# Performance work log

Hardware: AMD Instinct MI355X
Metric: run time of the kernel (lower is better)

## Reference

```python
import jax, jax.numpy as jnp
import numpy as np

DIM = 256
K = 255
PAD = K // 2  # 127, 'same' padding


def _dwconv(x, w, b, pad_h, pad_w):
    # x: [N, C, H, W]; w: [C, 1, kh, kw] (OIHW with feature_group_count=C)
    y = jax.lax.conv_general_dilated(
        x, w,
        window_strides=(1, 1),
        padding=((pad_h, pad_h), (pad_w, pad_w)),
        dimension_numbers=("NCHW", "OIHW", "NCHW"),
        feature_group_count=x.shape[1],
    )
    return y + b[None, :, None, None]


def setup_inputs() -> dict:
    key = jax.random.key(0)
    k1, k2, k3, k4, k5 = jax.random.split(key, 5)
    x = jax.random.normal(k1, (10, DIM, 128, 128), dtype=jnp.float32)
    # depthwise weights, scaled like torch's kaiming-uniform fan_in=K
    scale = 1.0 / np.sqrt(K)
    wh = jax.random.uniform(k2, (DIM, 1, K, 1), jnp.float32, -scale, scale)
    bh = jax.random.uniform(k3, (DIM,), jnp.float32, -scale, scale)
    ww = jax.random.uniform(k4, (DIM, 1, 1, K), jnp.float32, -scale, scale)
    bw = jax.random.uniform(k5, (DIM,), jnp.float32, -scale, scale)
    return {"x": x, "wh": wh, "bh": bh, "ww": ww, "bw": bw}


def reference(x, wh, bh, ww, bw):
    # conv_h: (K,1) depthwise conv, padding (K//2, 0)
    x = _dwconv(x, wh, bh, PAD, 0)
    # conv_w: (1,K) depthwise conv, padding (0, K//2)
    x = _dwconv(x, ww, bw, 0, PAD)
    return x
```

## Files before the change

### kernel.cpp

```cpp
#include <hip/hip_runtime.h>

#define HW 128
#define KTAPS 255
#define DIMC 256

typedef short short8 __attribute__((ext_vector_type(8)));
typedef float f32x16 __attribute__((ext_vector_type(16)));

__device__ __forceinline__ short f2bf(float f) {
    return __builtin_bit_cast(short, (__bf16)f);
}
__device__ __forceinline__ int pad16(int c) { return c + (c >> 3); }

__device__ __forceinline__ void bar_lds() {
    asm volatile("s_waitcnt lgkmcnt(0)" ::: "memory");
    __builtin_amdgcn_s_barrier();
}


__global__ __launch_bounds__(1024, 4)
void sep_conv255_mfma(const float* __restrict__ x,
                      const float* __restrict__ wh,
                      const float* __restrict__ bh,
                      const float* __restrict__ ww,
                      const float* __restrict__ bw,
                      float* __restrict__ out,
                      int nslices) {
    __shared__ __align__(16) short Px[2][2304 * 8];
    __shared__ __align__(16) short Py[2304 * 8];
    __shared__ __align__(16) short WB[1792 * 8];

    const int c    = blockIdx.x;
    const int tid  = threadIdx.x;
    const int lane = tid & 63;
    const int wv   = tid >> 6;
    const int wm   = wv >> 2;
    const int wn   = wv & 3;
    const int s31  = lane & 31;

    const float* __restrict__ whc = wh + c * KTAPS;
    const float* __restrict__ wwc = ww + c * KTAPS;
    const float bhv = bh[c];
    const float bwv = bw[c];

    const int xn   = tid & 127;
    const int xg   = tid >> 7;
    const int xch0 = (((xn >> 5) << 3) + xg) * 64 + (xn & 31);
    const size_t xoff = (size_t)(xg << 4) * HW + xn;

    float xv[16];
    {
        const float* xs = x + (size_t)c * (HW * HW);
#pragma unroll
        for (int i = 0; i < 16; ++i) xv[i] = xs[xoff + i * HW];
    }
#pragma unroll
    for (int i = 0; i < 2; ++i) {
        const int ch = tid + (i << 10);
        if (ch < 1792) {
            const int isB = (ch >= 896);
            const int lc  = ch & 63;
            const int t   = (ch >> 6) - (isB ? 14 : 0);
            const float* ws = isB ? wwc : whc;
            const float* wp = ws + (31 + (t << 4) + ((lc >> 5) << 3) - (lc & 31));
            short8 v;
#pragma unroll
            for (int j = 0; j < 8; ++j) v[j] = f2bf(wp[j]);
            *reinterpret_cast<short8*>(&WB[ch * 8]) = v;
        }
    }
#pragma unroll
    for (int hh = 0; hh < 2; ++hh) {
        short8 v;
#pragma unroll
        for (int j = 0; j < 8; ++j) v[j] = f2bf(xv[(hh << 3) + j]);
        *reinterpret_cast<short8*>(&Px[0][pad16(xch0 + (hh << 5)) * 8]) = v;
    }
    if (1 < nslices) {
        const float* xs = x + ((size_t)DIMC + c) * (HW * HW);
#pragma unroll
        for (int i = 0; i < 16; ++i) xv[i] = xs[xoff + i * HW];
    }
    bar_lds();

    const int hbase = (wm << 5) + ((lane >> 5) << 2);
    const int kk    = (wn << 5) + s31;
    const int ycb   = ((wm << 3) + (kk >> 4)) * 64 + (((kk >> 3) & 1) << 5);
    const int yjj   = kk & 7;

    for (int s = 0; s < nslices; ++s) {
        const int p = s & 1;

        f32x16 acc;
#pragma unroll
        for (int j = 0; j < 16; ++j) acc[j] = 0.0f;
#pragma unroll
        for (int ks = 0; ks < 8; ++ks) {
            const short8 a = *reinterpret_cast<const short8*>(
                &WB[(((ks - (wm << 1) + 6) << 6) + lane) * 8]);
            const short8 b = *reinterpret_cast<const short8*>(
                &Px[p][pad16(((wn << 3) + ks) * 64 + lane) * 8]);
            acc = __builtin_amdgcn_mfma_f32_32x32x16_bf16(a, b, acc, 0, 0, 0);
        }

#pragma unroll
        for (int r = 0; r < 16; ++r) {
            const int h = hbase + (r & 3) + ((r >> 2) << 3);
            Py[pad16(ycb + (h & 31)) * 8 + yjj] = f2bf(acc[r] + bhv);
        }

        if (s + 1 < nslices) {
#pragma unroll
            for (int hh = 0; hh < 2; ++hh) {
                short8 v;
#pragma unroll
                for (int j = 0; j < 8; ++j) v[j] = f2bf(xv[(hh << 3) + j]);
                *reinterpret_cast<short8*>(&Px[p ^ 1][pad16(xch0 + (hh << 5)) * 8]) = v;
            }
        }
        bar_lds();

        if (s + 2 < nslices) {
            const float* xs = x + ((size_t)(s + 2) * DIMC + c) * (HW * HW);
#pragma unroll
            for (int i = 0; i < 16; ++i) xv[i] = xs[xoff + i * HW];
        }

#pragma unroll
        for (int j = 0; j < 16; ++j) acc[j] = 0.0f;
#pragma unroll
        for (int ks = 0; ks < 8; ++ks) {
            const short8 a = *reinterpret_cast<const short8*>(
                &Py[pad16(((wm << 3) + ks) * 64 + lane) * 8]);
            const short8 b = *reinterpret_cast<const short8*>(
                &WB[(((ks - (wn << 1) + 20) << 6) + lane) * 8]);
            acc = __builtin_amdgcn_mfma_f32_32x32x16_bf16(a, b, acc, 0, 0, 0);
        }

        {
            float* zc = out + ((size_t)s * DIMC + c) * (HW * HW);
#pragma unroll
            for (int r = 0; r < 16; ++r) {
                const int h = hbase + (r & 3) + ((r >> 2) << 3);
                zc[(size_t)h * HW + kk] = acc[r] + bwv;
            }
        }
        bar_lds();
    }
}

extern "C" void kernel_launch(void* const* d_in, const int* in_sizes, int n_in,
                              void* d_out, int out_size, void* d_ws, size_t ws_size,
                              hipStream_t stream) {
    const float* x  = (const float*)d_in[0];
    const float* wh = (const float*)d_in[1];
    const float* bh = (const float*)d_in[2];
    const float* ww = (const float*)d_in[3];
    const float* bw = (const float*)d_in[4];
    float* outp = (float*)d_out;

    const int nbatch = in_sizes[0] / (DIMC * HW * HW);
    dim3 grid(DIMC);
    dim3 block(1024);
    hipLaunchKernelGGL(sep_conv255_mfma, grid, block, 0, stream,
                       x, wh, bh, ww, bw, outp, nbatch);
}
```

Before: 296.7 us.

## Swap conv order, fold biases, vectorize loads and stage stores via LDS

Runs the width convolution first and the height convolution second. The first-stage bias is folded into a per-column constant (bh times the sum of valid ww taps, plus bw) added once at the end. Input loads become float4 row loads, and output is transposed through an LDS tile so each thread does 16-byte coalesced global stores. The cost is more barriers per slice, a single-buffered input tile and extra LDS use, which may reduce overlap between loading and compute.

```diff
diff --git a/kernel.cpp b/kernel.cpp
--- a/kernel.cpp
+++ b/kernel.cpp
@@ -4,8 +4,10 @@
 #define KTAPS 255
 #define DIMC 256
 
-typedef short short8 __attribute__((ext_vector_type(8)));
-typedef float f32x16 __attribute__((ext_vector_type(16)));
+typedef short short8  __attribute__((ext_vector_type(8)));
+typedef short short4v __attribute__((ext_vector_type(4)));
+typedef float f32x16  __attribute__((ext_vector_type(16)));
+typedef float f32x4   __attribute__((ext_vector_type(4)));
 
 __device__ __forceinline__ short f2bf(float f) {
     return __builtin_bit_cast(short, (__bf16)f);
@@ -26,9 +28,11 @@
                       const float* __restrict__ bw,
                       float* __restrict__ out,
                       int nslices) {
-    __shared__ __align__(16) short Px[2][2304 * 8];
-    __shared__ __align__(16) short Py[2304 * 8];
-    __shared__ __align__(16) short WB[1792 * 8];
+    __shared__ __align__(16) short PxA[2304 * 8];
+    __shared__ __align__(16) short Py [2304 * 8];
+    __shared__ __align__(16) short WB [1792 * 8];
+    __shared__ __align__(16) float Zt [64 * 132];
+    __shared__ float cw[HW];
 
     const int c    = blockIdx.x;
     const int tid  = threadIdx.x;
@@ -37,22 +41,26 @@
     const int wm   = wv >> 2;
     const int wn   = wv & 3;
     const int s31  = lane & 31;
+    const int hi   = lane >> 5;
 
     const float* __restrict__ whc = wh + c * KTAPS;
     const float* __restrict__ wwc = ww + c * KTAPS;
-    const float bhv = bh[c];
-    const float bwv = bw[c];
-
-    const int xn   = tid & 127;
-    const int xg   = tid >> 7;
-    const int xch0 = (((xn >> 5) << 3) + xg) * 64 + (xn & 31);
-    const size_t xoff = (size_t)(xg << 4) * HW + xn;
-
-    float xv[16];
+
+    const int tw  = tid & 31;
+    const int bh0 = tid >> 5;
+    int stChunk[4];
+#pragma unroll
+    for (int i = 0; i < 4; ++i)
+        stChunk[i] = ((i << 3) + (tw >> 2)) * 64 + bh0 + (((tw >> 1) & 1) << 5);
+    const int stOff = (tw & 1) << 2;
+    const size_t ldOff = (size_t)bh0 * HW + (tw << 2);
+
+    f32x4 xv[4];
     {
         const float* xs = x + (size_t)c * (HW * HW);
 #pragma unroll
-        for (int i = 0; i < 16; ++i) xv[i] = xs[xoff + i * HW];
+        for (int i = 0; i < 4; ++i)
+            xv[i] = *reinterpret_cast<const f32x4*>(&xs[ldOff + (size_t)(i << 5) * HW]);
     }
 #pragma unroll
     for (int i = 0; i < 2; ++i) {
@@ -69,29 +77,67 @@
             *reinterpret_cast<short8*>(&WB[ch * 8]) = v;
         }
     }
-#pragma unroll
-    for (int hh = 0; hh < 2; ++hh) {
-        short8 v;
-#pragma unroll
-        for (int j = 0; j < 8; ++j) v[j] = f2bf(xv[(hh << 3) + j]);
-        *reinterpret_cast<short8*>(&Px[0][pad16(xch0 + (hh << 5)) * 8]) = v;
+    if (tid < HW) {
+        float s = 0.0f;
+        for (int i = 0; i < HW; ++i) s += wwc[127 - tid + i];
+        cw[tid] = bh[c] * s + bw[c];
+    }
+#pragma unroll
+    for (int i = 0; i < 4; ++i) {
+        short4v v;
+#pragma unroll
+        for (int j = 0; j < 4; ++j) v[j] = f2bf(xv[i][j]);
+        *reinterpret_cast<short4v*>(&PxA[pad16(stChunk[i]) * 8 + stOff]) = v;
     }
     if (1 < nslices) {
         const float* xs = x + ((size_t)DIMC + c) * (HW * HW);
 #pragma unroll
-        for (int i = 0; i < 16; ++i) xv[i] = xs[xoff + i * HW];
+        for (int i = 0; i < 4; ++i)
+            xv[i] = *reinterpret_cast<const f32x4*>(&xs[ldOff + (size_t)(i << 5) * HW]);
     }
     bar_lds();
 
-    const int hbase = (wm << 5) + ((lane >> 5) << 2);
-    const int kk    = (wn << 5) + s31;
-    const int ycb   = ((wm << 3) + (kk >> 4)) * 64 + (((kk >> 3) & 1) << 5);
-    const int yjj   = kk & 7;
+    const int   kk     = (wn << 5) + s31;
+    const float cwv    = cw[kk];
+    const int   hbase  = (wm << 5) + (hi << 2);
+    const int   rpBase = ((wn << 3) + (wm << 1)) * 64 + s31;
 
     for (int s = 0; s < nslices; ++s) {
-        const int p = s & 1;
-
         f32x16 acc;
+#pragma unroll
+        for (int j = 0; j < 16; ++j) acc[j] = 0.0f;
+#pragma unroll
+        for (int ks = 0; ks < 8; ++ks) {
+            const short8 a = *reinterpret_cast<const short8*>(
+                &PxA[pad16(((wm << 3) + ks) * 64 + lane) * 8]);
+            const short8 b = *reinterpret_cast<const short8*>(
+                &WB[(((ks - (wn << 1) + 20) << 6) + lane) * 8]);
+            acc = __builtin_amdgcn_mfma_f32_32x32x16_bf16(a, b, acc, 0, 0, 0);
+        }
+#pragma unroll
+        for (int r = 0; r < 16; ++r) {
+            const int chunk = rpBase + ((r >> 3) << 6) + (((r >> 2) & 1) << 5);
+            const int j     = (hi << 2) + (r & 3);
+            Py[pad16(chunk) * 8 + j] = f2bf(acc[r]);
+        }
+        bar_lds();
+
+        if (s + 1 < nslices) {
+#pragma unroll
+            for (int i = 0; i < 4; ++i) {
+                short4v v;
+#pragma unroll
+                for (int j = 0; j < 4; ++j) v[j] = f2bf(xv[i][j]);
+                *reinterpret_cast<short4v*>(&PxA[pad16(stChunk[i]) * 8 + stOff]) = v;
+            }
+        }
+        if (s + 2 < nslices) {
+            const float* xs = x + ((size_t)(s + 2) * DIMC + c) * (HW * HW);
+#pragma unroll
+            for (int i = 0; i < 4; ++i)
+                xv[i] = *reinterpret_cast<const f32x4*>(&xs[ldOff + (size_t)(i << 5) * HW]);
+        }
+
 #pragma unroll
         for (int j = 0; j < 16; ++j) acc[j] = 0.0f;
 #pragma unroll
@@ -99,53 +145,41 @@
             const short8 a = *reinterpret_cast<const short8*>(
                 &WB[(((ks - (wm << 1) + 6) << 6) + lane) * 8]);
             const short8 b = *reinterpret_cast<const short8*>(
-                &Px[p][pad16(((wn << 3) + ks) * 64 + lane) * 8]);
+                &Py[pad16(((wn << 3) + ks) * 64 + lane) * 8]);
             acc = __builtin_amdgcn_mfma_f32_32x32x16_bf16(a, b, acc, 0, 0, 0);
         }
 
-#pragma unroll
-        for (int r = 0; r < 16; ++r) {
-            const int h = hbase + (r & 3) + ((r >> 2) << 3);
-            Py[pad16(ycb + (h & 31)) * 8 + yjj] = f2bf(acc[r] + bhv);
-        }
-
-        if (s + 1 < nslices) {
-#pragma unroll
-            for (int hh = 0; hh < 2; ++hh) {
-                short8 v;
-#pragma unroll
-                for (int j = 0; j < 8; ++j) v[j] = f2bf(xv[(hh << 3) + j]);
-                *reinterpret_cast<short8*>(&Px[p ^ 1][pad16(xch0 + (hh << 5)) * 8]) = v;
-            }
-        }
-        bar_lds();
-
-        if (s + 2 < nslices) {
-            const float* xs = x + ((size_t)(s + 2) * DIMC + c) * (HW * HW);
-#pragma unroll
-            for (int i = 0; i < 16; ++i) xv[i] = xs[xoff + i * HW];
-        }
-
-#pragma unroll
-        for (int j = 0; j < 16; ++j) acc[j] = 0.0f;
-#pragma unroll
-        for (int ks = 0; ks < 8; ++ks) {
-            const short8 a = *reinterpret_cast<const short8*>(
-                &Py[pad16(((wm << 3) + ks) * 64 + lane) * 8]);
-            const short8 b = *reinterpret_cast<const short8*>(
-                &WB[(((ks - (wn << 1) + 20) << 6) + lane) * 8]);
-            acc = __builtin_amdgcn_mfma_f32_32x32x16_bf16(a, b, acc, 0, 0, 0);
-        }
-
-        {
-            float* zc = out + ((size_t)s * DIMC + c) * (HW * HW);
+        float* zc = out + ((size_t)s * DIMC + c) * (HW * HW);
+
+        if (wm < 2) {
 #pragma unroll
             for (int r = 0; r < 16; ++r) {
                 const int h = hbase + (r & 3) + ((r >> 2) << 3);
-                zc[(size_t)h * HW + kk] = acc[r] + bwv;
+                Zt[h * 132 + kk] = acc[r] + cwv;
             }
         }
         bar_lds();
+#pragma unroll
+        for (int i = 0; i < 2; ++i) {
+            const int hh = bh0 + (i << 5);
+            const f32x4 v = *reinterpret_cast<const f32x4*>(&Zt[hh * 132 + (tw << 2)]);
+            *reinterpret_cast<f32x4*>(&zc[(size_t)hh * HW + (tw << 2)]) = v;
+        }
+        bar_lds();
+        if (wm >= 2) {
+#pragma unroll
+            for (int r = 0; r < 16; ++r) {
+                const int h = hbase + (r & 3) + ((r >> 2) << 3);
+                Zt[(h - 64) * 132 + kk] = acc[r] + cwv;
+            }
+        }
+        bar_lds();
+#pragma unroll
+        for (int i = 0; i < 2; ++i) {
+            const int hh = bh0 + (i << 5);
+            const f32x4 v = *reinterpret_cast<const f32x4*>(&Zt[hh * 132 + (tw << 2)]);
+            *reinterpret_cast<f32x4*>(&zc[(size_t)(64 + hh) * HW + (tw << 2)]) = v;
+        }
     }
 }
 
```

Result: no change. 291.1 us (-1.9%).
